# Kernel optimization log

Hardware: AMD Instinct MI355X
Metric: run time of the kernel (lower is better)

Reference implementation:

```python
import jax, jax.numpy as jnp
import numpy as np

B, SL, H = 8, 512, 768
NS, W = 256, 32            # num_spans, max_span_width (static pad width)
NH = 12
HD = H // NH
FFN_I = int(H * 4)         # int(output_dim * ffn_ratio)
LN_EPS = 1e-5
NEG = -1e9


def _pos_encoding(seq_len, hidden):
    pos = jnp.arange(seq_len, dtype=jnp.float32)[:, None]
    div = jnp.exp(jnp.arange(0, hidden, 2, dtype=jnp.float32) * (-np.log(10000.0) / hidden))
    pe = jnp.zeros((seq_len, hidden), jnp.float32)
    pe = pe.at[:, 0::2].set(jnp.sin(pos * div))
    pe = pe.at[:, 1::2].set(jnp.cos(pos * div))
    return pe


def _layernorm(x, g, b):
    mu = jnp.mean(x, axis=-1, keepdims=True)
    var = jnp.mean(jnp.square(x - mu), axis=-1, keepdims=True)
    return (x - mu) * jax.lax.rsqrt(var + LN_EPS) * g + b


def setup_inputs() -> dict:
    key = jax.random.key(0)
    ks = jax.random.split(key, 16)
    token_reps = jax.random.normal(ks[0], (B, SL, H), jnp.float32)
    starts = jax.random.randint(ks[1], (B, NS), 0, SL - W)
    widths = jax.random.randint(ks[2], (B, NS), 0, W + 1)  # includes empty spans
    span_ids = jnp.stack([starts, starts + widths], axis=-1).astype(jnp.int64)
    s = 0.02
    return {
        "token_reps": token_reps,
        "span_ids": span_ids,
        "dummy_query": jax.random.normal(ks[3], (1, 1, H), jnp.float32),
        "in_proj_w": jax.random.normal(ks[4], (3 * H, H), jnp.float32) * s,
        "in_proj_b": jnp.zeros((3 * H,), jnp.float32),
        "out_proj_w": jax.random.normal(ks[5], (H, H), jnp.float32) * s,
        "out_proj_b": jnp.zeros((H,), jnp.float32),
        "ln_g": jnp.ones((H,), jnp.float32),
        "ln_b": jnp.zeros((H,), jnp.float32),
        "ffn_w1": jax.random.normal(ks[6], (FFN_I, H), jnp.float32) * s,
        "ffn_b1": jnp.zeros((FFN_I,), jnp.float32),
        "ffn_w2": jax.random.normal(ks[7], (H, FFN_I), jnp.float32) * s,
        "ffn_b2": jnp.zeros((H,), jnp.float32),
        "pooling": 1,
    }


def reference(token_reps, span_ids, dummy_query, in_proj_w, in_proj_b,
              out_proj_w, out_proj_b, ln_g, ln_b,
              ffn_w1, ffn_b1, ffn_w2, ffn_b2, pooling):
    # sequence positional encoding (dropout=0 / eval mode)
    pe = _pos_encoding(SL, H)
    tok = token_reps + pe[None, :, :]

    starts = span_ids[..., 0]                        # (B, NS)
    lengths = span_ids[..., 1] - span_ids[..., 0]    # (B, NS)
    offs = jnp.arange(W)
    pos = starts[..., None] + offs                   # (B, NS, W)
    valid = offs[None, None, :] < lengths[..., None] # (B, NS, W) bool
    idx = jnp.clip(pos, 0, SL - 1)
    # vectorized span gather -> padded tensor (B, NS, W, H), zeros on padding
    spans = tok[jnp.arange(B)[:, None, None], idx]
    spans = spans * valid[..., None].astype(tok.dtype)

    N = B * NS
    spans = spans.reshape(N, W, H)
    valid_f = valid.reshape(N, W)

    Wq, Wk, Wv = jnp.split(in_proj_w, 3, axis=0)
    bq, bk, bv = jnp.split(in_proj_b, 3, axis=0)

    q0 = dummy_query[0, 0]                            # (H,)
    q = (q0 @ Wq.T + bq).reshape(NH, HD)              # (NH, HD)
    k = (spans @ Wk.T + bk).reshape(N, W, NH, HD)
    v = (spans @ Wv.T + bv).reshape(N, W, NH, HD)

    scores = jnp.einsum('hd,nwhd->nhw', q, k) / np.sqrt(HD)
    scores = jnp.where(valid_f[:, None, :], scores, NEG)
    attn = jax.nn.softmax(scores, axis=-1)            # (N, NH, W)
    ctx = jnp.einsum('nhw,nwhd->nhd', attn, v).reshape(N, H)
    attn_out = ctx @ out_proj_w.T + out_proj_b        # (N, H)

    x = _layernorm(attn_out + q0, ln_g, ln_b)
    h = jnp.maximum(x @ ffn_w1.T + ffn_b1, 0.0)
    x = _layernorm((h @ ffn_w2.T + ffn_b2) + x, ln_g, ln_b)

    out = x.reshape(B, NS, H)
    out = jnp.where((lengths > 0)[..., None], out, 0.0)
    return out
```

## Files before the change

### kernel.cpp

```cpp
#include <hip/hip_runtime.h>
#include <hip/hip_bf16.h>
#include <cstdint>

#define Bb 8
#define SLh 512
#define Hh 768
#define NSs 256
#define Ww 32
#define NHh 12
#define HDd 64
#define FFN_I 3072
#define NTOK (Bb*SLh)
#define NSPAN (Bb*NSs)

typedef __attribute__((ext_vector_type(8))) __bf16 bf16x8;
typedef __attribute__((ext_vector_type(4))) float f32x4;

__device__ __forceinline__ short f2bf(float f) {
  unsigned u = __builtin_bit_cast(unsigned, f);
  unsigned r = (u + 0x7fffu + ((u >> 16) & 1u)) >> 16;
  return (short)r;
}
__device__ __forceinline__ float bflo(unsigned u) { return __builtin_bit_cast(float, u << 16); }
__device__ __forceinline__ float bfhi(unsigned u) { return __builtin_bit_cast(float, u & 0xffff0000u); }

__device__ __forceinline__ void gload16(const void* g, void* l) {
  __builtin_amdgcn_global_load_lds(
      (__attribute__((address_space(1))) void*)(const_cast<void*>(g)),
      (__attribute__((address_space(3))) void*)l, 16, 0, 0);
}

__global__ __launch_bounds__(192) void tok_kernel(const float* __restrict__ tr,
                                                  short* __restrict__ tok) {
  int row = blockIdx.x;
  int s = row & (SLh - 1);
  int c0 = threadIdx.x * 4;
  float4 v = *(const float4*)(tr + (size_t)row * Hh + c0);
  const float kinv = -9.210340371976184f / (float)Hh;
  float f0 = __expf((float)c0 * kinv);
  float f1 = __expf((float)(c0 + 2) * kinv);
  float s0, cc0, s1, cc1;
  __sincosf((float)s * f0, &s0, &cc0);
  __sincosf((float)s * f1, &s1, &cc1);
  v.x += s0; v.y += cc0; v.z += s1; v.w += cc1;
  short4 o{f2bf(v.x), f2bf(v.y), f2bf(v.z), f2bf(v.w)};
  *(short4*)(tok + (size_t)row * Hh + c0) = o;
}

__global__ __launch_bounds__(256) void cast4(const float* __restrict__ s0,
                                             const float* __restrict__ s1,
                                             const float* __restrict__ s2,
                                             const float* __restrict__ s3,
                                             short* __restrict__ d0,
                                             short* __restrict__ d1,
                                             short* __restrict__ d2,
                                             short* __restrict__ d3) {
  int b = blockIdx.x;
  const float* s; short* d; int off;
  if (b < 1152)      { s = s0; d = d0; off = b; }
  else if (b < 1728) { s = s1; d = d1; off = b - 1152; }
  else if (b < 4032) { s = s2; d = d2; off = b - 1728; }
  else               { s = s3; d = d3; off = b - 4032; }
  int i = off * 256 + threadIdx.x;
  float4 v = ((const float4*)s)[i];
  short4 o{f2bf(v.x), f2bf(v.y), f2bf(v.z), f2bf(v.w)};
  ((short4*)d)[i] = o;
}

__global__ __launch_bounds__(64) void prep_qb(const float* __restrict__ dq,
                                              const float* __restrict__ ipw,
                                              const float* __restrict__ ipb,
                                              const float* __restrict__ opb,
                                              float* __restrict__ qsv,
                                              float* __restrict__ bias2) {
  int h = blockIdx.x * 64 + threadIdx.x;
  const float4* wr = (const float4*)(ipw + (size_t)h * Hh);
  const float4* qv = (const float4*)dq;
  float acc = 0.f;
  for (int j = 0; j < Hh / 4; ++j) {
    float4 w4 = wr[j], q4 = qv[j];
    acc += w4.x * q4.x + w4.y * q4.y + w4.z * q4.z + w4.w * q4.w;
  }
  acc += ipb[h];
  qsv[h] = acc * 0.125f;
  bias2[h] = opb[h] + dq[h];
}

template <int EPI>
__global__ __launch_bounds__(256, 3) void gemm_bt(const short* __restrict__ A,
                                                  const short* __restrict__ Bt,
                                                  const float* __restrict__ bias,
                                                  float* __restrict__ Cf,
                                                  short* __restrict__ Cb,
                                                  int M, int N, int ldk, int Kc) {
  __shared__ __align__(16) char Al[2][128 * 128];
  __shared__ __align__(16) char Bl[2][64 * 128];
  const int tid = threadIdx.x;
  const int lane = tid & 63, wave = tid >> 6;
  const int wm = wave >> 1, wn = wave & 1;
  const int row0 = blockIdx.y * 128, col0 = blockIdx.x * 64;
  const int kbase = blockIdx.z * Kc;
  const int l15 = lane & 15, hi = lane >> 4;
  f32x4 acc[4][2] = {};
  const int nk = Kc >> 6;
  const int srow = tid >> 3, sslot = tid & 7;

  auto stage = [&](int kt, int bi) {
    const short* Agp = A + (size_t)row0 * ldk + kbase + kt * 64;
    const short* Bgp = Bt + (size_t)col0 * ldk + kbase + kt * 64;
#pragma unroll
    for (int j = 0; j < 4; ++j) {
      int row = j * 32 + srow;
      int col = (sslot ^ (row & 7)) << 3;
      gload16(Agp + (size_t)row * ldk + col,
              &Al[bi][0] + (size_t)(j * 256 + wave * 64) * 16);
    }
#pragma unroll
    for (int j = 0; j < 2; ++j) {
      int row = j * 32 + srow;
      int col = (sslot ^ (row & 7)) << 3;
      gload16(Bgp + (size_t)row * ldk + col,
              &Bl[bi][0] + (size_t)(j * 256 + wave * 64) * 16);
    }
  };

  stage(0, 0);
  for (int kt = 0; kt < nk; ++kt) {
    const int cur = kt & 1;
    if (kt + 1 < nk) {
      stage(kt + 1, cur ^ 1);
      asm volatile("s_waitcnt vmcnt(6)" ::: "memory");
    } else {
      asm volatile("s_waitcnt vmcnt(0)" ::: "memory");
    }
    __builtin_amdgcn_s_barrier();
    asm volatile("" ::: "memory");
    bf16x8 fa[2][4], fb[2][2];
#pragma unroll
    for (int kk = 0; kk < 2; ++kk) {
#pragma unroll
      for (int i = 0; i < 4; ++i) {
        int Ra = wm * 64 + i * 16 + l15;
        fa[kk][i] = *(const bf16x8*)(&Al[cur][0] + (size_t)Ra * 128 +
                                     (((kk * 4 + hi) ^ (Ra & 7)) << 4));
      }
#pragma unroll
      for (int i = 0; i < 2; ++i) {
        int Rb = wn * 32 + i * 16 + l15;
        fb[kk][i] = *(const bf16x8*)(&Bl[cur][0] + (size_t)Rb * 128 +
                                     (((kk * 4 + hi) ^ (Rb & 7)) << 4));
      }
    }
#pragma unroll
    for (int kk = 0; kk < 2; ++kk)
#pragma unroll
      for (int mi = 0; mi < 4; ++mi)
#pragma unroll
        for (int ni = 0; ni < 2; ++ni)
          acc[mi][ni] = __builtin_amdgcn_mfma_f32_16x16x32_bf16(fa[kk][mi], fb[kk][ni], acc[mi][ni], 0, 0, 0);
    asm volatile("" ::: "memory");
    __builtin_amdgcn_s_barrier();
  }

  float* dst = (EPI == 3) ? (Cf + (size_t)blockIdx.z * M * N) : Cf;
#pragma unroll
  for (int mi = 0; mi < 4; ++mi) {
#pragma unroll
    for (int ni = 0; ni < 2; ++ni) {
      int colb = col0 + wn * 32 + ni * 16 + l15;
      float bv = (EPI == 3) ? 0.f : bias[colb];
#pragma unroll
      for (int r = 0; r < 4; ++r) {
        int rowb = row0 + wm * 64 + mi * 16 + hi * 4 + r;
        float v = acc[mi][ni][r] + bv;
        if (EPI == 1) v = fmaxf(v, 0.f);
        if (EPI == 3) {
          dst[(size_t)rowb * N + colb] = v;
        } else {
          Cb[(size_t)rowb * N + colb] = f2bf(v);
        }
      }
    }
  }
}

__global__ __launch_bounds__(384) void attn_kernel(const short* __restrict__ KV,
                                                   const int* __restrict__ sid,
                                                   const float* __restrict__ qs,
                                                   short* __restrict__ ctx) {
  int n = blockIdx.x;
  int b = n >> 8;
  __shared__ int posO[Ww];
  __shared__ float attnL[NHh][Ww];
  __shared__ int lenS;
  int tid = threadIdx.x;
  if (tid < Ww) {
    int st = sid[2 * n], en = sid[2 * n + 1];
    int p = st + tid;
    p = p < 0 ? 0 : (p > SLh - 1 ? SLh - 1 : p);
    posO[tid] = (b * SLh + p) * (2 * Hh);
    if (tid == 0) lenS = en - st;
  }
  __syncthreads();
  int len = lenS;
  int h = tid >> 5, w = tid & 31;
  const int4* kr = (const int4*)(KV + posO[w] + h * HDd);
  const float4* qp = (const float4*)(qs + h * HDd);
  float acc = 0.f;
#pragma unroll
  for (int j = 0; j < 8; ++j) {
    int4 kk = kr[j];
    float4 qa = qp[2 * j], qb = qp[2 * j + 1];
    acc += qa.x * bflo(kk.x) + qa.y * bfhi(kk.x) + qa.z * bflo(kk.y) + qa.w * bfhi(kk.y);
    acc += qb.x * bflo(kk.z) + qb.y * bfhi(kk.z) + qb.z * bflo(kk.w) + qb.w * bfhi(kk.w);
  }
  float score = (w < len) ? acc : -1e9f;
  float m = score;
#pragma unroll
  for (int o = 16; o; o >>= 1) m = fmaxf(m, __shfl_xor(m, o, 32));
  float e = __expf(score - m);
  float ssum = e;
#pragma unroll
  for (int o = 16; o; o >>= 1) ssum += __shfl_xor(ssum, o, 32);
  attnL[h][w] = e / ssum;
  __syncthreads();
  int hh = tid >> 5, dp = tid & 31;
  float a0 = 0.f, a1 = 0.f;
#pragma unroll
  for (int w2 = 0; w2 < Ww; ++w2) {
    float aw = attnL[hh][w2];
    unsigned u = *(const unsigned*)(KV + posO[w2] + Hh + hh * HDd + 2 * dp);
    a0 += aw * bflo(u);
    a1 += aw * bfhi(u);
  }
  unsigned packed = (unsigned)(unsigned short)f2bf(a0) | ((unsigned)(unsigned short)f2bf(a1) << 16);
  ((unsigned*)ctx)[(size_t)n * (Hh / 2) + tid] = packed;
}

__global__ __launch_bounds__(256) void ln_kernel(const float* __restrict__ Y4,
                                                 const float* __restrict__ bias2,
                                                 const float* __restrict__ g,
                                                 const float* __restrict__ b,
                                                 float* __restrict__ xf,
                                                 short* __restrict__ xb) {
  const size_t SL = (size_t)NSPAN * Hh;
  int row = blockIdx.x;
  int tid = threadIdx.x;
  float v[3]; float s1 = 0.f, s2 = 0.f;
#pragma unroll
  for (int i = 0; i < 3; ++i) {
    int c = tid + 256 * i;
    size_t idx = (size_t)row * Hh + c;
    v[i] = Y4[idx] + Y4[idx + SL] + Y4[idx + 2 * SL] + Y4[idx + 3 * SL] + bias2[c];
    s1 += v[i]; s2 += v[i] * v[i];
  }
  __shared__ float r1[4], r2[4];
#pragma unroll
  for (int o = 32; o; o >>= 1) { s1 += __shfl_xor(s1, o); s2 += __shfl_xor(s2, o); }
  int lane = tid & 63, wv = tid >> 6;
  if (lane == 0) { r1[wv] = s1; r2[wv] = s2; }
  __syncthreads();
  s1 = r1[0] + r1[1] + r1[2] + r1[3];
  s2 = r2[0] + r2[1] + r2[2] + r2[3];
  float mu = s1 * (1.f / Hh);
  float var = s2 * (1.f / Hh) - mu * mu;
  float is = rsqrtf(var + 1e-5f);
#pragma unroll
  for (int i = 0; i < 3; ++i) {
    int c = tid + 256 * i;
    float o = (v[i] - mu) * is * g[c] + b[c];
    xf[(size_t)row * Hh + c] = o;
    xb[(size_t)row * Hh + c] = f2bf(o);
  }
}

__global__ __launch_bounds__(256) void ln_final(const float* __restrict__ Y4,
                                                const float* __restrict__ b2,
                                                const float* __restrict__ xf,
                                                const float* __restrict__ g,
                                                const float* __restrict__ b,
                                                const int* __restrict__ sid,
                                                float* __restrict__ out) {
  const size_t SL = (size_t)NSPAN * Hh;
  int row = blockIdx.x;
  int len = sid[2 * row + 1] - sid[2 * row];
  int tid = threadIdx.x;
  float v[3]; float s1 = 0.f, s2 = 0.f;
#pragma unroll
  for (int i = 0; i < 3; ++i) {
    int c = tid + 256 * i;
    size_t idx = (size_t)row * Hh + c;
    v[i] = Y4[idx] + Y4[idx + SL] + Y4[idx + 2 * SL] + Y4[idx + 3 * SL]
         + b2[c] + xf[idx];
    s1 += v[i]; s2 += v[i] * v[i];
  }
  __shared__ float r1[4], r2[4];
#pragma unroll
  for (int o = 32; o; o >>= 1) { s1 += __shfl_xor(s1, o); s2 += __shfl_xor(s2, o); }
  int lane = tid & 63, wv = tid >> 6;
  if (lane == 0) { r1[wv] = s1; r2[wv] = s2; }
  __syncthreads();
  s1 = r1[0] + r1[1] + r1[2] + r1[3];
  s2 = r2[0] + r2[1] + r2[2] + r2[3];
  float mu = s1 * (1.f / Hh);
  float var = s2 * (1.f / Hh) - mu * mu;
  float is = rsqrtf(var + 1e-5f);
  float keep = (len > 0) ? 1.f : 0.f;
#pragma unroll
  for (int i = 0; i < 3; ++i) {
    int c = tid + 256 * i;
    float o = ((v[i] - mu) * is * g[c] + b[c]) * keep;
    out[(size_t)row * Hh + c] = o;
  }
}

extern "C" void kernel_launch(void* const* d_in, const int* in_sizes, int n_in,
                              void* d_out, int out_size, void* d_ws, size_t ws_size,
                              hipStream_t stream) {
  const float* token_reps = (const float*)d_in[0];
  const int* span_ids = (const int*)d_in[1];
  const float* dq = (const float*)d_in[2];
  const float* ipw = (const float*)d_in[3];
  const float* ipb = (const float*)d_in[4];
  const float* opw = (const float*)d_in[5];
  const float* opb = (const float*)d_in[6];
  const float* lng = (const float*)d_in[7];
  const float* lnb = (const float*)d_in[8];
  const float* w1 = (const float*)d_in[9];
  const float* b1 = (const float*)d_in[10];
  const float* w2 = (const float*)d_in[11];
  const float* b2 = (const float*)d_in[12];
  float* out = (float*)d_out;

  char* p = (char*)d_ws;
  auto alloc = [&](size_t bytes) { void* r = p; p += (bytes + 255) & ~(size_t)255; return r; };
  short* tokb = (short*)alloc((size_t)NTOK * Hh * 2);
  short* kvw  = (short*)alloc((size_t)2 * Hh * Hh * 2);
  short* outw = (short*)alloc((size_t)Hh * Hh * 2);
  short* w1b  = (short*)alloc((size_t)FFN_I * Hh * 2);
  short* w2b  = (short*)alloc((size_t)Hh * FFN_I * 2);
  float* qsv  = (float*)alloc(Hh * 4);
  float* bias2= (float*)alloc(Hh * 4);
  short* KV   = (short*)alloc((size_t)NTOK * 2 * Hh * 2);
  short* ctxb = (short*)alloc((size_t)NSPAN * Hh * 2);
  float* attnY= (float*)alloc((size_t)4 * NSPAN * Hh * 4);
  float* xf   = (float*)alloc((size_t)NSPAN * Hh * 4);
  short* xb   = (short*)alloc((size_t)NSPAN * Hh * 2);
  short* hb   = (short*)alloc((size_t)NSPAN * FFN_I * 2);
  float* y2   = (float*)alloc((size_t)4 * NSPAN * Hh * 4);

  tok_kernel<<<NTOK, 192, 0, stream>>>(token_reps, tokb);
  cast4<<<6336, 256, 0, stream>>>(ipw + (size_t)Hh * Hh, opw, w1, w2,
                                  kvw, outw, w1b, w2b);
  prep_qb<<<12, 64, 0, stream>>>(dq, ipw, ipb, opb, qsv, bias2);
  gemm_bt<0><<<dim3(24, 32, 1), 256, 0, stream>>>(tokb, kvw, ipb + Hh,
                                                  nullptr, KV,
                                                  NTOK, 2 * Hh, Hh, Hh);
  attn_kernel<<<NSPAN, 384, 0, stream>>>(KV, span_ids, qsv, ctxb);
  gemm_bt<3><<<dim3(12, 16, 4), 256, 0, stream>>>(ctxb, outw, nullptr,
                                                  attnY, nullptr,
                                                  NSPAN, Hh, Hh, Hh / 4);
  ln_kernel<<<NSPAN, 256, 0, stream>>>(attnY, bias2, lng, lnb, xf, xb);
  gemm_bt<1><<<dim3(48, 16, 1), 256, 0, stream>>>(xb, w1b, b1,
                                                  nullptr, hb,
                                                  NSPAN, FFN_I, Hh, Hh);
  gemm_bt<3><<<dim3(12, 16, 4), 256, 0, stream>>>(hb, w2b, nullptr,
                                                  y2, nullptr,
                                                  NSPAN, Hh, FFN_I, FFN_I / 4);
  ln_final<<<NSPAN, 256, 0, stream>>>(y2, b2, xf, lng, lnb, span_ids, out);
}
```

Baseline: 234.8 us.

## Fold query into key weights to replace K projection with per-head score columns

```diff
diff --git a/kernel.cpp b/kernel.cpp
--- a/kernel.cpp
+++ b/kernel.cpp
@@ -12,6 +12,7 @@
 #define FFN_I 3072
 #define NTOK (Bb*SLh)
 #define NSPAN (Bb*NSs)
+#define NVS 832
 
 typedef __attribute__((ext_vector_type(8))) __bf16 bf16x8;
 typedef __attribute__((ext_vector_type(4))) float f32x4;
@@ -56,11 +57,16 @@
                                              short* __restrict__ d2,
                                              short* __restrict__ d3) {
   int b = blockIdx.x;
+  if (b >= 5760) {
+    int i = (b - 5760) * 256 + threadIdx.x;
+    ((short4*)d0)[149760 + i] = short4{0, 0, 0, 0};
+    return;
+  }
   const float* s; short* d; int off;
-  if (b < 1152)      { s = s0; d = d0; off = b; }
-  else if (b < 1728) { s = s1; d = d1; off = b - 1152; }
-  else if (b < 4032) { s = s2; d = d2; off = b - 1728; }
-  else               { s = s3; d = d3; off = b - 4032; }
+  if (b < 576)       { s = s0; d = d0; off = b; }
+  else if (b < 1152) { s = s1; d = d1; off = b - 576; }
+  else if (b < 3456) { s = s2; d = d2; off = b - 1152; }
+  else               { s = s3; d = d3; off = b - 3456; }
   int i = off * 256 + threadIdx.x;
   float4 v = ((const float4*)s)[i];
   short4 o{f2bf(v.x), f2bf(v.y), f2bf(v.z), f2bf(v.w)};
@@ -72,8 +78,11 @@
                                               const float* __restrict__ ipb,
                                               const float* __restrict__ opb,
                                               float* __restrict__ qsv,
-                                              float* __restrict__ bias2) {
-  int h = blockIdx.x * 64 + threadIdx.x;
+                                              float* __restrict__ bias2,
+                                              float* __restrict__ bvs) {
+  int b = blockIdx.x, lane = threadIdx.x;
+  if (b == 12) { if (lane < 52) bvs[780 + lane] = 0.f; return; }
+  int h = b * 64 + lane;
   const float4* wr = (const float4*)(ipw + (size_t)h * Hh);
   const float4* qv = (const float4*)dq;
   float acc = 0.f;
@@ -82,8 +91,27 @@
     acc += w4.x * q4.x + w4.y * q4.y + w4.z * q4.z + w4.w * q4.w;
   }
   acc += ipb[h];
-  qsv[h] = acc * 0.125f;
+  float qs = acc * 0.125f;
+  qsv[h] = qs;
   bias2[h] = opb[h] + dq[h];
+  bvs[h] = ipb[2 * Hh + h];
+  float t = qs * ipb[Hh + h];
+#pragma unroll
+  for (int o = 32; o; o >>= 1) t += __shfl_xor(t, o);
+  if (lane == 0) bvs[768 + b] = t;
+}
+
+__global__ __launch_bounds__(64) void qk_kernel(const float* __restrict__ ipw,
+                                                const float* __restrict__ qsv,
+                                                short* __restrict__ vsw) {
+  int h = blockIdx.x, dc = blockIdx.y, lane = threadIdx.x;
+  int d = dc * 64 + lane;
+  const float* wk = ipw + (size_t)(Hh + h * 64) * Hh + d;
+  const float* qh = qsv + h * 64;
+  float a = 0.f;
+#pragma unroll 8
+  for (int e = 0; e < 64; ++e) a += qh[e] * wk[(size_t)e * Hh];
+  vsw[(size_t)(768 + h) * Hh + d] = f2bf(a);
 }
 
 template <int EPI>
@@ -92,14 +120,18 @@
                                                   const float* __restrict__ bias,
                                                   float* __restrict__ Cf,
                                                   short* __restrict__ Cb,
-                                                  int M, int N, int ldk, int Kc) {
+                                                  int M, int N, int ldk, int Kc,
+                                                  int nx, int ypp) {
   __shared__ __align__(16) char Al[2][128 * 128];
   __shared__ __align__(16) char Bl[2][64 * 128];
   const int tid = threadIdx.x;
   const int lane = tid & 63, wave = tid >> 6;
   const int wm = wave >> 1, wn = wave & 1;
-  const int row0 = blockIdx.y * 128, col0 = blockIdx.x * 64;
-  const int kbase = blockIdx.z * Kc;
+  const int bid = blockIdx.x, xcd = bid & 7, ii = bid >> 3;
+  const int iy = ii / nx;
+  const int by = xcd * ypp + iy, bx = ii - iy * nx;
+  const int row0 = by * 128, col0 = bx * 64;
+  const int kbase = blockIdx.y * Kc;
   const int l15 = lane & 15, hi = lane >> 4;
   f32x4 acc[4][2] = {};
   const int nk = Kc >> 6;
@@ -162,7 +194,7 @@
     __builtin_amdgcn_s_barrier();
   }
 
-  float* dst = (EPI == 3) ? (Cf + (size_t)blockIdx.z * M * N) : Cf;
+  float* dst = (EPI == 3) ? (Cf + (size_t)blockIdx.y * M * N) : Cf;
 #pragma unroll
   for (int mi = 0; mi < 4; ++mi) {
 #pragma unroll
@@ -173,24 +205,26 @@
       for (int r = 0; r < 4; ++r) {
         int rowb = row0 + wm * 64 + mi * 16 + hi * 4 + r;
         float v = acc[mi][ni][r] + bv;
-        if (EPI == 1) v = fmaxf(v, 0.f);
-        if (EPI == 3) {
+        if (EPI == 1) {
+          Cb[(size_t)rowb * N + colb] = f2bf(fmaxf(v, 0.f));
+        } else if (EPI == 3) {
           dst[(size_t)rowb * N + colb] = v;
         } else {
-          Cb[(size_t)rowb * N + colb] = f2bf(v);
+          if (colb < 768) Cb[(size_t)rowb * 768 + colb] = f2bf(v);
+          else if (colb < 780) Cf[(size_t)rowb * 12 + (colb - 768)] = v;
         }
       }
     }
   }
 }
 
-__global__ __launch_bounds__(384) void attn_kernel(const short* __restrict__ KV,
+__global__ __launch_bounds__(384) void attn_kernel(const short* __restrict__ Vb,
+                                                   const float* __restrict__ S,
                                                    const int* __restrict__ sid,
-                                                   const float* __restrict__ qs,
                                                    short* __restrict__ ctx) {
   int n = blockIdx.x;
   int b = n >> 8;
-  __shared__ int posO[Ww];
+  __shared__ int posV[Ww], tS[Ww];
   __shared__ float attnL[NHh][Ww];
   __shared__ int lenS;
   int tid = threadIdx.x;
@@ -198,23 +232,15 @@
     int st = sid[2 * n], en = sid[2 * n + 1];
     int p = st + tid;
     p = p < 0 ? 0 : (p > SLh - 1 ? SLh - 1 : p);
-    posO[tid] = (b * SLh + p) * (2 * Hh);
+    int t = b * SLh + p;
+    posV[tid] = t * Hh;
+    tS[tid] = t * 12;
     if (tid == 0) lenS = en - st;
   }
   __syncthreads();
   int len = lenS;
   int h = tid >> 5, w = tid & 31;
-  const int4* kr = (const int4*)(KV + posO[w] + h * HDd);
-  const float4* qp = (const float4*)(qs + h * HDd);
-  float acc = 0.f;
-#pragma unroll
-  for (int j = 0; j < 8; ++j) {
-    int4 kk = kr[j];
-    float4 qa = qp[2 * j], qb = qp[2 * j + 1];
-    acc += qa.x * bflo(kk.x) + qa.y * bfhi(kk.x) + qa.z * bflo(kk.y) + qa.w * bfhi(kk.y);
-    acc += qb.x * bflo(kk.z) + qb.y * bfhi(kk.z) + qb.z * bflo(kk.w) + qb.w * bfhi(kk.w);
-  }
-  float score = (w < len) ? acc : -1e9f;
+  float score = (w < len) ? S[tS[w] + h] : -1e9f;
   float m = score;
 #pragma unroll
   for (int o = 16; o; o >>= 1) m = fmaxf(m, __shfl_xor(m, o, 32));
@@ -229,7 +255,7 @@
 #pragma unroll
   for (int w2 = 0; w2 < Ww; ++w2) {
     float aw = attnL[hh][w2];
-    unsigned u = *(const unsigned*)(KV + posO[w2] + Hh + hh * HDd + 2 * dp);
+    unsigned u = *(const unsigned*)(Vb + posV[w2] + hh * HDd + 2 * dp);
     a0 += aw * bflo(u);
     a1 += aw * bfhi(u);
   }
@@ -237,7 +263,7 @@
   ((unsigned*)ctx)[(size_t)n * (Hh / 2) + tid] = packed;
 }
 
-__global__ __launch_bounds__(256) void ln_kernel(const float* __restrict__ Y4,
+__global__ __launch_bounds__(256) void ln_kernel(const float* __restrict__ Y2,
                                                  const float* __restrict__ bias2,
                                                  const float* __restrict__ g,
                                                  const float* __restrict__ b,
@@ -251,7 +277,7 @@
   for (int i = 0; i < 3; ++i) {
     int c = tid + 256 * i;
     size_t idx = (size_t)row * Hh + c;
-    v[i] = Y4[idx] + Y4[idx + SL] + Y4[idx + 2 * SL] + Y4[idx + 3 * SL] + bias2[c];
+    v[i] = Y2[idx] + Y2[idx + SL] + bias2[c];
     s1 += v[i]; s2 += v[i] * v[i];
   }
   __shared__ float r1[4], r2[4];
@@ -335,37 +361,36 @@
   char* p = (char*)d_ws;
   auto alloc = [&](size_t bytes) { void* r = p; p += (bytes + 255) & ~(size_t)255; return r; };
   short* tokb = (short*)alloc((size_t)NTOK * Hh * 2);
-  short* kvw  = (short*)alloc((size_t)2 * Hh * Hh * 2);
+  short* vsw  = (short*)alloc((size_t)NVS * Hh * 2);
   short* outw = (short*)alloc((size_t)Hh * Hh * 2);
   short* w1b  = (short*)alloc((size_t)FFN_I * Hh * 2);
   short* w2b  = (short*)alloc((size_t)Hh * FFN_I * 2);
   float* qsv  = (float*)alloc(Hh * 4);
   float* bias2= (float*)alloc(Hh * 4);
-  short* KV   = (short*)alloc((size_t)NTOK * 2 * Hh * 2);
+  float* bvs  = (float*)alloc(NVS * 4);
+  float* S    = (float*)alloc((size_t)NTOK * 12 * 4);
+  short* Vb   = (short*)alloc((size_t)NTOK * Hh * 2);
   short* ctxb = (short*)alloc((size_t)NSPAN * Hh * 2);
-  float* attnY= (float*)alloc((size_t)4 * NSPAN * Hh * 4);
+  float* attnY= (float*)alloc((size_t)2 * NSPAN * Hh * 4);
   float* xf   = (float*)alloc((size_t)NSPAN * Hh * 4);
   short* xb   = (short*)alloc((size_t)NSPAN * Hh * 2);
   short* hb   = (short*)alloc((size_t)NSPAN * FFN_I * 2);
   float* y2   = (float*)alloc((size_t)4 * NSPAN * Hh * 4);
 
   tok_kernel<<<NTOK, 192, 0, stream>>>(token_reps, tokb);
-  cast4<<<6336, 256, 0, stream>>>(ipw + (size_t)Hh * Hh, opw, w1, w2,
-                                  kvw, outw, w1b, w2b);
-  prep_qb<<<12, 64, 0, stream>>>(dq, ipw, ipb, opb, qsv, bias2);
-  gemm_bt<0><<<dim3(24, 32, 1), 256, 0, stream>>>(tokb, kvw, ipb + Hh,
-                                                  nullptr, KV,
-                                                  NTOK, 2 * Hh, Hh, Hh);
-  attn_kernel<<<NSPAN, 384, 0, stream>>>(KV, span_ids, qsv, ctxb);
-  gemm_bt<3><<<dim3(12, 16, 4), 256, 0, stream>>>(ctxb, outw, nullptr,
-                                                  attnY, nullptr,
-                                                  NSPAN, Hh, Hh, Hh / 4);
+  cast4<<<5799, 256, 0, stream>>>(ipw + (size_t)2 * Hh * Hh, opw, w1, w2,
+                                  vsw, outw, w1b, w2b);
+  prep_qb<<<13, 64, 0, stream>>>(dq, ipw, ipb, opb, qsv, bias2, bvs);
+  qk_kernel<<<dim3(12, 12), 64, 0, stream>>>(ipw, qsv, vsw);
+  gemm_bt<4><<<dim3(416, 1), 256, 0, stream>>>(tokb, vsw, bvs, S, Vb,
+                                               NTOK, NVS, Hh, Hh, 13, 4);
+  attn_kernel<<<NSPAN, 384, 0, stream>>>(Vb, S, span_ids, ctxb);
+  gemm_bt<3><<<dim3(192, 2), 256, 0, stream>>>(ctxb, outw, nullptr, attnY, nullptr,
+                                               NSPAN, Hh, Hh, Hh / 2, 12, 2);
   ln_kernel<<<NSPAN, 256, 0, stream>>>(attnY, bias2, lng, lnb, xf, xb);
-  gemm_bt<1><<<dim3(48, 16, 1), 256, 0, stream>>>(xb, w1b, b1,
-                                                  nullptr, hb,
-                                                  NSPAN, FFN_I, Hh, Hh);
-  gemm_bt<3><<<dim3(12, 16, 4), 256, 0, stream>>>(hb, w2b, nullptr,
-                                                  y2, nullptr,
-                                                  NSPAN, Hh, FFN_I, FFN_I / 4);
+  gemm_bt<1><<<dim3(768, 1), 256, 0, stream>>>(xb, w1b, b1, nullptr, hb,
+                                               NSPAN, FFN_I, Hh, Hh, 48, 2);
+  gemm_bt<3><<<dim3(192, 4), 256, 0, stream>>>(hb, w2b, nullptr, y2, nullptr,
+                                               NSPAN, Hh, FFN_I, FFN_I / 4, 12, 2);
   ln_final<<<NSPAN, 256, 0, stream>>>(y2, b2, xf, lng, lnb, span_ids, out);
 }
```

New measurement: 210.3 us. 10.4% less time.
